# Optimization experiments

Hardware: AMD Instinct MI355X
Metric: run time of the kernel (lower is better)

## Reference

```python
import jax, jax.numpy as jnp
import numpy as np

T, D = 8192, 256   # frames, feature dim
P, K = 64, 128     # phone vocabulary, centers per phone


def setup_inputs() -> dict:
    key = jax.random.key(0)
    k1, k2, k3 = jax.random.split(key, 3)
    h = jax.random.normal(k1, (T, D), dtype=jnp.float32)
    centers = jax.random.normal(k2, (P, K, D), dtype=jnp.float32)
    phones = jax.random.randint(k3, (T,), 0, P, dtype=jnp.int64)
    return {"h": h, "centers": centers, "phones": phones}


def reference(h, centers, phones):
    """Per-phone 1-NN retrieval: for each frame t, find nearest center in the
    pool for phones[t] and return that center (anonymized feature).
    centers: [P, K, D] padded table replacing the (pattern, phone, gender) dict.
    """
    c = centers[phones]                                # [T, K, D] irregular gather
    # squared euclidean distance; ||h_t||^2 is constant per row -> omit for argmin
    d2 = jnp.sum(c * c, axis=-1) - 2.0 * jnp.einsum("td,tkd->tk", h, c)  # [T, K]
    idx = jnp.argmin(d2, axis=-1)                      # [T]
    h_anon = jnp.take_along_axis(c, idx[:, None, None], axis=1)[:, 0, :]  # [T, D]
    return h_anon
```

## Files before the change

kernel.cpp:

```cpp
#include <hip/hip_runtime.h>

#define T_FRAMES 8192
#define D_DIM    256
#define P_PHONES 64
#define K_CENT   128
#define TILE_F   32
#define BUCKET_CAP 256
#define SLOTS_PP   8
#define MAX_SLOTS  (P_PHONES * SLOTS_PP)
#define MARGIN   1.0f

#define WS_NORMS  0
#define WS_FIDX   32768
#define WS_DESC   98304
#define WS_HH     106496
#define WS_CH     (106496 + 4194304)

typedef _Float16 half8 __attribute__((ext_vector_type(8)));
typedef float    f32x4 __attribute__((ext_vector_type(4)));

__global__ __launch_bounds__(1024) void qr_prep_kernel(const float* __restrict__ h,
                                                       const float* __restrict__ centers,
                                                       const int* __restrict__ phones,
                                                       float* __restrict__ norms,
                                                       int* __restrict__ fidx,
                                                       int4* __restrict__ desc,
                                                       _Float16* __restrict__ hH,
                                                       _Float16* __restrict__ cH) {
    const int b   = blockIdx.x;
    const int tid = threadIdx.x;

    if (b < 512) {
        const size_t e = ((size_t)b * 1024 + tid) * 4;
        union { _Float16 hf[4]; uint2 u; } pk;
        float4 v = *(const float4*)(h + e);
        pk.hf[0] = (_Float16)v.x; pk.hf[1] = (_Float16)v.y;
        pk.hf[2] = (_Float16)v.z; pk.hf[3] = (_Float16)v.w;
        *(uint2*)(hH + e) = pk.u;
        v = *(const float4*)(centers + e);
        pk.hf[0] = (_Float16)v.x; pk.hf[1] = (_Float16)v.y;
        pk.hf[2] = (_Float16)v.z; pk.hf[3] = (_Float16)v.w;
        *(uint2*)(cH + e) = pk.u;
        float s = v.x * v.x + v.y * v.y + v.z * v.z + v.w * v.w;
#pragma unroll
        for (int off = 32; off; off >>= 1) s += __shfl_xor(s, off, 64);
        if ((tid & 63) == 0) norms[b * 16 + (tid >> 6)] = s;
        return;
    }

    __shared__ int nsh;
    const int j    = b - 512;
    const int w    = tid >> 6;
    const int lane = tid & 63;
    if (tid == 0) nsh = 0;
    __syncthreads();

    for (int ch = 0; ch < 8; ++ch) {
        const int f = w * 512 + ch * 64 + lane;
        const bool mt = (phones[f] == j);
        const unsigned long long mask = __ballot(mt);
        const int cnt = __popcll(mask);
        int base = 0;
        if (cnt) {
            if (lane == 0) base = atomicAdd(&nsh, cnt);
            base = __shfl(base, 0, 64);
            if (mt) {
                const int pos = base + __popcll(mask & ((1ull << lane) - 1ull));
                if (pos < BUCKET_CAP) fidx[j * BUCKET_CAP + pos] = f;
            }
        }
    }
    __syncthreads();

    if (tid == 0) {
        const int c = nsh > BUCKET_CAP ? BUCKET_CAP : nsh;
#pragma unroll
        for (int k = 0; k < SLOTS_PP; ++k) {
            const int rem = c - k * TILE_F;
            const int fc  = rem < 0 ? 0 : (rem > TILE_F ? TILE_F : rem);
            desc[j * SLOTS_PP + k] = make_int4(j, j * BUCKET_CAP + k * TILE_F, fc, 0);
        }
    }
}

__global__ __launch_bounds__(256) void qr_main_kernel(const float* __restrict__ h,
                                                      const float* __restrict__ centers,
                                                      const float* __restrict__ norms,
                                                      const int* __restrict__ fidx,
                                                      const int4* __restrict__ desc,
                                                      const _Float16* __restrict__ hH,
                                                      const _Float16* __restrict__ cH,
                                                      float* __restrict__ out) {
    __shared__ float d2s[TILE_F * K_CENT];
    __shared__ float mins[TILE_F];
    __shared__ int   cnt[TILE_F];
    __shared__ short cand[TILE_F * 32];
    __shared__ int   widx[TILE_F];
    __shared__ int   rlist[TILE_F];
    __shared__ int   rn;

    const int4 dsc = desc[blockIdx.x];
    const int fcnt = dsc.z;
    if (fcnt == 0) return;
    const int p = dsc.x, fstart = dsc.y;

    const int tid  = threadIdx.x;
    const int wave = tid >> 6;
    const int lane = tid & 63;
    const int m    = lane & 15;
    const int quad = lane >> 4;

    if (tid < TILE_F) cnt[tid] = 0;
    if (tid == 0) rn = 0;

    half8 aF[2][8];
#pragma unroll
    for (int t = 0; t < 2; ++t) {
        const int fiA = fidx[fstart + min(t * 16 + m, fcnt - 1)];
        const _Float16* ap = hH + (size_t)fiA * D_DIM + quad * 8;
#pragma unroll
        for (int s = 0; s < 8; ++s) aF[t][s] = *(const half8*)(ap + s * 32);
    }

#pragma unroll
    for (int u = 0; u < 2; ++u) {
        const int c = (wave * 2 + u) * 16 + m;
        const _Float16* bp = cH + ((size_t)p * K_CENT + c) * D_DIM + quad * 8;
        half8 bF[8];
#pragma unroll
        for (int s = 0; s < 8; ++s) bF[s] = *(const half8*)(bp + s * 32);
        f32x4 acc0 = {0.f, 0.f, 0.f, 0.f};
        f32x4 acc1 = {0.f, 0.f, 0.f, 0.f};
#pragma unroll
        for (int s = 0; s < 8; ++s) {
            acc0 = __builtin_amdgcn_mfma_f32_16x16x32_f16(aF[0][s], bF[s], acc0, 0, 0, 0);
            acc1 = __builtin_amdgcn_mfma_f32_16x16x32_f16(aF[1][s], bF[s], acc1, 0, 0, 0);
        }
        const float nrm = norms[p * K_CENT + c];
#pragma unroll
        for (int r = 0; r < 4; ++r) {
            d2s[(quad * 4 + r) * K_CENT + c]        = nrm - 2.0f * acc0[r];
            d2s[(16 + quad * 4 + r) * K_CENT + c]   = nrm - 2.0f * acc1[r];
        }
    }
    __syncthreads();

    const int fr = tid >> 3;
    const int g  = tid & 7;
    float v[16];
    {
        float mn = 3.0e38f;
#pragma unroll
        for (int jx = 0; jx < 16; ++jx) {
            v[jx] = d2s[fr * K_CENT + g * 16 + jx];
            mn = fminf(mn, v[jx]);
        }
        mn = fminf(mn, __shfl_xor(mn, 1, 64));
        mn = fminf(mn, __shfl_xor(mn, 2, 64));
        mn = fminf(mn, __shfl_xor(mn, 4, 64));
        if (g == 0) mins[fr] = mn;
    }
    __syncthreads();

    {
        const float tau = mins[fr] + MARGIN;
#pragma unroll
        for (int jx = 0; jx < 16; ++jx) {
            if (v[jx] < tau) {
                const int pos = atomicAdd(&cnt[fr], 1);
                if (pos < 32) cand[fr * 32 + pos] = (short)(g * 16 + jx);
            }
        }
    }
    __syncthreads();

    if (tid < TILE_F && tid < fcnt) {
        if (cnt[tid] == 1) widx[tid] = (int)cand[tid * 32];
        else rlist[atomicAdd(&rn, 1)] = tid;
    }
    __syncthreads();

    for (int r = wave; r < rn; r += 4) {
        const int f2 = rlist[r];
        const int fi = fidx[fstart + f2];
        const float4 hv = ((const float4*)(h + (size_t)fi * D_DIM))[lane];
        const int n = cnt[f2];
        const int ncand = (n <= 32) ? n : K_CENT;
        float best = 3.0e38f; int bc = 0x7FFFFFFF;
        for (int ci = 0; ci < ncand; ++ci) {
            const int c = (n <= 32) ? (int)cand[f2 * 32 + ci] : ci;
            const float4 cv = ((const float4*)(centers + ((size_t)p * K_CENT + c) * D_DIM))[lane];
            float s = hv.x * cv.x + hv.y * cv.y + hv.z * cv.z + hv.w * cv.w;
#pragma unroll
            for (int off = 32; off; off >>= 1) s += __shfl_xor(s, off, 64);
            const float d2 = norms[p * K_CENT + c] - 2.0f * s;
            if (d2 < best || (d2 == best && c < bc)) { best = d2; bc = c; }
        }
        if (lane == 0) widx[f2] = bc;
    }
    __syncthreads();

    if (fr < fcnt) {
        const int fo = fidx[fstart + fr];
        const float4* src = (const float4*)(centers + ((size_t)p * K_CENT + widx[fr]) * D_DIM);
        float4* dst = (float4*)(out + (size_t)fo * D_DIM);
#pragma unroll
        for (int jx = 0; jx < 8; ++jx) dst[g + 8 * jx] = src[g + 8 * jx];
    }
}

extern "C" void kernel_launch(void* const* d_in, const int* in_sizes, int n_in,
                              void* d_out, int out_size, void* d_ws, size_t ws_size,
                              hipStream_t stream) {
    const float* h       = (const float*)d_in[0];
    const float* centers = (const float*)d_in[1];
    const int*   phones  = (const int*)d_in[2];
    float*       out     = (float*)d_out;

    char* ws = (char*)d_ws;
    float*     norms = (float*)(ws + WS_NORMS);
    int*       fidx  = (int*)(ws + WS_FIDX);
    int4*      desc  = (int4*)(ws + WS_DESC);
    _Float16*  hH    = (_Float16*)(ws + WS_HH);
    _Float16*  cH    = (_Float16*)(ws + WS_CH);

    qr_prep_kernel<<<576, 1024, 0, stream>>>(h, centers, phones, norms, fidx, desc, hH, cH);
    qr_main_kernel<<<MAX_SLOTS, 256, 0, stream>>>(h, centers, norms, fidx, desc, hH, cH, out);
}
```

Baseline: 88.75 us.

## Fuse prep and main kernels into one with in-block bucketing and fp16 conversion

Removes the separate prep kernel. Each block now scans the phones array itself, builds its phone bucket through a ballot and prefix scan in shared memory, converts h and centers to fp16 on the fly, and computes center norms locally. This drops a kernel launch, the workspace round trip, and the full fp16 copies of h and centers. The cost is redundant work: every block of the same phone rescans all 8192 phones and recomputes the same norms and conversions.

```diff
diff --git a/kernel.cpp b/kernel.cpp
--- a/kernel.cpp
+++ b/kernel.cpp
@@ -7,91 +7,22 @@
 #define TILE_F   32
 #define BUCKET_CAP 256
 #define SLOTS_PP   8
-#define MAX_SLOTS  (P_PHONES * SLOTS_PP)
+#define NBLOCKS  (P_PHONES * SLOTS_PP)
 #define MARGIN   1.0f
-
-#define WS_NORMS  0
-#define WS_FIDX   32768
-#define WS_DESC   98304
-#define WS_HH     106496
-#define WS_CH     (106496 + 4194304)
 
 typedef _Float16 half8 __attribute__((ext_vector_type(8)));
 typedef float    f32x4 __attribute__((ext_vector_type(4)));
 
-__global__ __launch_bounds__(1024) void qr_prep_kernel(const float* __restrict__ h,
-                                                       const float* __restrict__ centers,
-                                                       const int* __restrict__ phones,
-                                                       float* __restrict__ norms,
-                                                       int* __restrict__ fidx,
-                                                       int4* __restrict__ desc,
-                                                       _Float16* __restrict__ hH,
-                                                       _Float16* __restrict__ cH) {
-    const int b   = blockIdx.x;
-    const int tid = threadIdx.x;
-
-    if (b < 512) {
-        const size_t e = ((size_t)b * 1024 + tid) * 4;
-        union { _Float16 hf[4]; uint2 u; } pk;
-        float4 v = *(const float4*)(h + e);
-        pk.hf[0] = (_Float16)v.x; pk.hf[1] = (_Float16)v.y;
-        pk.hf[2] = (_Float16)v.z; pk.hf[3] = (_Float16)v.w;
-        *(uint2*)(hH + e) = pk.u;
-        v = *(const float4*)(centers + e);
-        pk.hf[0] = (_Float16)v.x; pk.hf[1] = (_Float16)v.y;
-        pk.hf[2] = (_Float16)v.z; pk.hf[3] = (_Float16)v.w;
-        *(uint2*)(cH + e) = pk.u;
-        float s = v.x * v.x + v.y * v.y + v.z * v.z + v.w * v.w;
-#pragma unroll
-        for (int off = 32; off; off >>= 1) s += __shfl_xor(s, off, 64);
-        if ((tid & 63) == 0) norms[b * 16 + (tid >> 6)] = s;
-        return;
-    }
-
-    __shared__ int nsh;
-    const int j    = b - 512;
-    const int w    = tid >> 6;
-    const int lane = tid & 63;
-    if (tid == 0) nsh = 0;
-    __syncthreads();
-
-    for (int ch = 0; ch < 8; ++ch) {
-        const int f = w * 512 + ch * 64 + lane;
-        const bool mt = (phones[f] == j);
-        const unsigned long long mask = __ballot(mt);
-        const int cnt = __popcll(mask);
-        int base = 0;
-        if (cnt) {
-            if (lane == 0) base = atomicAdd(&nsh, cnt);
-            base = __shfl(base, 0, 64);
-            if (mt) {
-                const int pos = base + __popcll(mask & ((1ull << lane) - 1ull));
-                if (pos < BUCKET_CAP) fidx[j * BUCKET_CAP + pos] = f;
-            }
-        }
-    }
-    __syncthreads();
-
-    if (tid == 0) {
-        const int c = nsh > BUCKET_CAP ? BUCKET_CAP : nsh;
-#pragma unroll
-        for (int k = 0; k < SLOTS_PP; ++k) {
-            const int rem = c - k * TILE_F;
-            const int fc  = rem < 0 ? 0 : (rem > TILE_F ? TILE_F : rem);
-            desc[j * SLOTS_PP + k] = make_int4(j, j * BUCKET_CAP + k * TILE_F, fc, 0);
-        }
-    }
-}
-
-__global__ __launch_bounds__(256) void qr_main_kernel(const float* __restrict__ h,
-                                                      const float* __restrict__ centers,
-                                                      const float* __restrict__ norms,
-                                                      const int* __restrict__ fidx,
-                                                      const int4* __restrict__ desc,
-                                                      const _Float16* __restrict__ hH,
-                                                      const _Float16* __restrict__ cH,
-                                                      float* __restrict__ out) {
+__global__ __launch_bounds__(256) void qr_all_kernel(const float* __restrict__ h,
+                                                     const float* __restrict__ centers,
+                                                     const int* __restrict__ phones,
+                                                     float* __restrict__ out) {
+    __shared__ int   gcnt[128];
+    __shared__ int   gpre[128];
+    __shared__ int   lfid[BUCKET_CAP];
+    __shared__ int   ctot_s;
     __shared__ float d2s[TILE_F * K_CENT];
+    __shared__ float nrm_s[K_CENT];
     __shared__ float mins[TILE_F];
     __shared__ int   cnt[TILE_F];
     __shared__ short cand[TILE_F * 32];
@@ -99,36 +30,95 @@
     __shared__ int   rlist[TILE_F];
     __shared__ int   rn;
 
-    const int4 dsc = desc[blockIdx.x];
-    const int fcnt = dsc.z;
-    if (fcnt == 0) return;
-    const int p = dsc.x, fstart = dsc.y;
-
+    const int b    = blockIdx.x;
+    const int p    = b >> 3;
+    const int k    = b & 7;
     const int tid  = threadIdx.x;
     const int wave = tid >> 6;
     const int lane = tid & 63;
+
+    for (int i = 0; i < 32; ++i) {
+        const int g = wave * 32 + i;
+        const unsigned long long mask = __ballot(phones[g * 64 + lane] == p);
+        if (lane == 0) gcnt[g] = __popcll(mask);
+    }
+    __syncthreads();
+
+    if (wave == 0) {
+        const int a0 = gcnt[lane], a1 = gcnt[64 + lane];
+        int s0 = a0, s1 = a1;
+#pragma unroll
+        for (int off = 1; off < 64; off <<= 1) {
+            int y = __shfl_up(s0, off, 64); if (lane >= off) s0 += y;
+            y = __shfl_up(s1, off, 64);     if (lane >= off) s1 += y;
+        }
+        s1 += __shfl(s0, 63, 64);
+        gpre[lane]      = s0 - a0;
+        gpre[64 + lane] = s1 - a1;
+        if (lane == 63) ctot_s = s1;
+    }
+    __syncthreads();
+    const int fcnt = min(TILE_F, min(ctot_s, BUCKET_CAP) - k * TILE_F);
+    if (fcnt <= 0) return;
+
+    for (int i = 0; i < 32; ++i) {
+        const int g = wave * 32 + i;
+        const int f = g * 64 + lane;
+        const bool mt = (phones[f] == p);
+        const unsigned long long mask = __ballot(mt);
+        if (mt) {
+            const int pos = gpre[g] + __popcll(mask & ((1ull << lane) - 1ull));
+            if (pos < BUCKET_CAP) lfid[pos] = f;
+        }
+    }
+    if (tid < TILE_F) cnt[tid] = 0;
+    if (tid == 0) rn = 0;
+    __syncthreads();
+
     const int m    = lane & 15;
     const int quad = lane >> 4;
 
-    if (tid < TILE_F) cnt[tid] = 0;
-    if (tid == 0) rn = 0;
-
     half8 aF[2][8];
 #pragma unroll
     for (int t = 0; t < 2; ++t) {
-        const int fiA = fidx[fstart + min(t * 16 + m, fcnt - 1)];
-        const _Float16* ap = hH + (size_t)fiA * D_DIM + quad * 8;
-#pragma unroll
-        for (int s = 0; s < 8; ++s) aF[t][s] = *(const half8*)(ap + s * 32);
+        const int fiA = lfid[k * TILE_F + min(t * 16 + m, fcnt - 1)];
+        const float* ap = h + (size_t)fiA * D_DIM + quad * 8;
+#pragma unroll
+        for (int s = 0; s < 8; ++s) {
+            const float4 x0 = *(const float4*)(ap + s * 32);
+            const float4 x1 = *(const float4*)(ap + s * 32 + 4);
+            half8 hh;
+            hh[0] = (_Float16)x0.x; hh[1] = (_Float16)x0.y;
+            hh[2] = (_Float16)x0.z; hh[3] = (_Float16)x0.w;
+            hh[4] = (_Float16)x1.x; hh[5] = (_Float16)x1.y;
+            hh[6] = (_Float16)x1.z; hh[7] = (_Float16)x1.w;
+            aF[t][s] = hh;
+        }
     }
 
 #pragma unroll
     for (int u = 0; u < 2; ++u) {
         const int c = (wave * 2 + u) * 16 + m;
-        const _Float16* bp = cH + ((size_t)p * K_CENT + c) * D_DIM + quad * 8;
+        const float* cp = centers + ((size_t)p * K_CENT + c) * D_DIM + quad * 8;
         half8 bF[8];
-#pragma unroll
-        for (int s = 0; s < 8; ++s) bF[s] = *(const half8*)(bp + s * 32);
+        float sq = 0.0f;
+#pragma unroll
+        for (int s = 0; s < 8; ++s) {
+            const float4 x0 = *(const float4*)(cp + s * 32);
+            const float4 x1 = *(const float4*)(cp + s * 32 + 4);
+            sq += x0.x * x0.x + x0.y * x0.y + x0.z * x0.z + x0.w * x0.w
+                + x1.x * x1.x + x1.y * x1.y + x1.z * x1.z + x1.w * x1.w;
+            half8 hb;
+            hb[0] = (_Float16)x0.x; hb[1] = (_Float16)x0.y;
+            hb[2] = (_Float16)x0.z; hb[3] = (_Float16)x0.w;
+            hb[4] = (_Float16)x1.x; hb[5] = (_Float16)x1.y;
+            hb[6] = (_Float16)x1.z; hb[7] = (_Float16)x1.w;
+            bF[s] = hb;
+        }
+        sq += __shfl_xor(sq, 16, 64);
+        sq += __shfl_xor(sq, 32, 64);
+        if (quad == 0) nrm_s[c] = sq;
+
         f32x4 acc0 = {0.f, 0.f, 0.f, 0.f};
         f32x4 acc1 = {0.f, 0.f, 0.f, 0.f};
 #pragma unroll
@@ -136,11 +126,10 @@
             acc0 = __builtin_amdgcn_mfma_f32_16x16x32_f16(aF[0][s], bF[s], acc0, 0, 0, 0);
             acc1 = __builtin_amdgcn_mfma_f32_16x16x32_f16(aF[1][s], bF[s], acc1, 0, 0, 0);
         }
-        const float nrm = norms[p * K_CENT + c];
 #pragma unroll
         for (int r = 0; r < 4; ++r) {
-            d2s[(quad * 4 + r) * K_CENT + c]        = nrm - 2.0f * acc0[r];
-            d2s[(16 + quad * 4 + r) * K_CENT + c]   = nrm - 2.0f * acc1[r];
+            d2s[(quad * 4 + r) * K_CENT + c]      = sq - 2.0f * acc0[r];
+            d2s[(16 + quad * 4 + r) * K_CENT + c] = sq - 2.0f * acc1[r];
         }
     }
     __syncthreads();
@@ -182,7 +171,7 @@
 
     for (int r = wave; r < rn; r += 4) {
         const int f2 = rlist[r];
-        const int fi = fidx[fstart + f2];
+        const int fi = lfid[k * TILE_F + f2];
         const float4 hv = ((const float4*)(h + (size_t)fi * D_DIM))[lane];
         const int n = cnt[f2];
         const int ncand = (n <= 32) ? n : K_CENT;
@@ -193,7 +182,7 @@
             float s = hv.x * cv.x + hv.y * cv.y + hv.z * cv.z + hv.w * cv.w;
 #pragma unroll
             for (int off = 32; off; off >>= 1) s += __shfl_xor(s, off, 64);
-            const float d2 = norms[p * K_CENT + c] - 2.0f * s;
+            const float d2 = nrm_s[c] - 2.0f * s;
             if (d2 < best || (d2 == best && c < bc)) { best = d2; bc = c; }
         }
         if (lane == 0) widx[f2] = bc;
@@ -201,7 +190,7 @@
     __syncthreads();
 
     if (fr < fcnt) {
-        const int fo = fidx[fstart + fr];
+        const int fo = lfid[k * TILE_F + fr];
         const float4* src = (const float4*)(centers + ((size_t)p * K_CENT + widx[fr]) * D_DIM);
         float4* dst = (float4*)(out + (size_t)fo * D_DIM);
 #pragma unroll
@@ -217,13 +206,5 @@
     const int*   phones  = (const int*)d_in[2];
     float*       out     = (float*)d_out;
 
-    char* ws = (char*)d_ws;
-    float*     norms = (float*)(ws + WS_NORMS);
-    int*       fidx  = (int*)(ws + WS_FIDX);
-    int4*      desc  = (int4*)(ws + WS_DESC);
-    _Float16*  hH    = (_Float16*)(ws + WS_HH);
-    _Float16*  cH    = (_Float16*)(ws + WS_CH);
-
-    qr_prep_kernel<<<576, 1024, 0, stream>>>(h, centers, phones, norms, fidx, desc, hH, cH);
-    qr_main_kernel<<<MAX_SLOTS, 256, 0, stream>>>(h, centers, norms, fidx, desc, hH, cH, out);
+    qr_all_kernel<<<NBLOCKS, 256, 0, stream>>>(h, centers, phones, out);
 }
```

Measured after the change: 101.0 us. 13.8% more time.
